# Optimization experiments

Measured on AMD Instinct MI355X. Metric: run time of the kernel, lower is better.

Reference implementation:

```python
import jax, jax.numpy as jnp
import numpy as np
import math

N_HEADS = 12  # from init_kwargs


def setup_inputs() -> dict:
    key = jax.random.key(0)
    ks = jax.random.split(key, 9)
    B, N, D = 32, 577, 768
    s = 1.0 / math.sqrt(D)
    return {
        "x": jax.random.normal(ks[0], (B, N, D), jnp.float32),
        "Wq": jax.random.normal(ks[1], (D, D), jnp.float32) * s,
        "bq": jax.random.normal(ks[2], (D,), jnp.float32) * 0.02,
        "Wk": jax.random.normal(ks[3], (D, D), jnp.float32) * s,
        "bk": jax.random.normal(ks[4], (D,), jnp.float32) * 0.02,
        "Wv": jax.random.normal(ks[5], (D, D), jnp.float32) * s,
        "bv": jax.random.normal(ks[6], (D,), jnp.float32) * 0.02,
        "Wo": jax.random.normal(ks[7], (D, D), jnp.float32) * s,
        "bo": jax.random.normal(ks[8], (D,), jnp.float32) * 0.02,
    }


def reference(x, Wq, bq, Wk, bk, Wv, bv, Wo, bo):
    B, N, D = x.shape
    H = N_HEADS
    Hd = D // H
    # project then split heads (intended semantics of the torch module)
    q = (x @ Wq.T + bq).reshape(B, N, H, Hd)
    k = (x @ Wk.T + bk).reshape(B, N, H, Hd)
    v = (x @ Wv.T + bv).reshape(B, N, H, Hd)
    # NOTE: faithful quirk - scale by sqrt(d_size), not sqrt(head_dim)
    scores = jnp.einsum('bqhd,bkhd->bhqk', q, k) / math.sqrt(D)  # [B,H,N,N]
    # faithful quirk: mask = triu(ones); positions where mask==0 (strictly
    # lower triangle, k < q) are filled with float32 min -> anti-causal mask
    allowed = jnp.triu(jnp.ones((N, N), dtype=bool))
    scores = jnp.where(allowed, scores, jnp.finfo(jnp.float32).min)
    att = jax.nn.softmax(scores, axis=3)  # dropout p=0.0 -> identity
    out = jnp.einsum('bhqk,bkhd->bqhd', att, v).reshape(B, N, D)
    return out @ Wo.T + bo
```

## Files before the change

### kernel.cpp

```cpp
#include <hip/hip_runtime.h>
#include <cstdint>
#include <cstddef>


typedef __bf16 bf16;
typedef __bf16 bf16x4 __attribute__((ext_vector_type(4)));
typedef __bf16 bf16x8 __attribute__((ext_vector_type(8)));
typedef float  f32x4  __attribute__((ext_vector_type(4)));

#define DEVI __device__ __forceinline__

constexpr int BATCH = 32;
constexpr int NSEQ  = 577;
constexpr int DMODEL= 768;
constexpr int NHEAD = 12;
constexpr int HD    = 64;
constexpr int M_ROWS = BATCH * NSEQ;
constexpr int M_PAD  = 145 * 128;
constexpr int N_PAD  = 640;
constexpr int QKV_N  = 3 * DMODEL;
constexpr float QSCALE = 0.036084391824351615f * 1.4426950408889634f;

DEVI void async_copy16(const void* g, void* l) {
  void* gg = (void*)(uintptr_t)g;
  __builtin_amdgcn_global_load_lds(
      (__attribute__((address_space(1))) void*)gg,
      (__attribute__((address_space(3))) void*)l,
      16, 0, 0);
}

DEVI f32x4 mfma16(bf16x8 a, bf16x8 b, f32x4 c) {
  return __builtin_amdgcn_mfma_f32_16x16x32_bf16(a, b, c, 0, 0, 0);
}

__global__ __launch_bounds__(256) void cast_kernel(
    const float* __restrict__ x,
    const float* __restrict__ wq, const float* __restrict__ wk,
    const float* __restrict__ wv, const float* __restrict__ wo,
    bf16* __restrict__ xb, bf16* __restrict__ wcat, bf16* __restrict__ wob)
{
  constexpr int XQ = (M_ROWS * DMODEL) / 4;
  constexpr int WQ = (DMODEL * DMODEL) / 4;
  int idx = blockIdx.x * 256 + threadIdx.x;
  const float4* src; bf16* dst; int off;
  if (idx < XQ) { src = (const float4*)x; dst = xb; off = idx; }
  else {
    int u = idx - XQ; int w = u / WQ; off = u - w * WQ;
    src = (const float4*)(w == 0 ? wq : w == 1 ? wk : w == 2 ? wv : wo);
    dst = (w < 3) ? (wcat + (size_t)w * DMODEL * DMODEL) : wob;
  }
  float4 v = src[off];
  bf16x4 o;
  o[0] = (bf16)v.x; o[1] = (bf16)v.y; o[2] = (bf16)v.z; o[3] = (bf16)v.w;
  *(bf16x4*)(dst + (size_t)off * 4) = o;
}

template <int MODE>
__global__ __launch_bounds__(256) void gemm_bt(
    const bf16* __restrict__ A, const bf16* __restrict__ Bw,
    const float* __restrict__ bias0, const float* __restrict__ bias1,
    const float* __restrict__ bias2,
    float* __restrict__ Cout,
    bf16* __restrict__ Qb, bf16* __restrict__ Kb, bf16* __restrict__ Vb)
{
  __shared__ __align__(16) char smem[65536];
  const int t = threadIdx.x;
  const int w = t >> 6, lane = t & 63;
  const int g = lane >> 4, cl = lane & 15;
  const int wm = (w >> 1) * 64, wn = (w & 1) * 64;

  constexpr int GX  = (MODE == 0 ? QKV_N : DMODEL) / 128;
  constexpr int NWG = GX * (M_PAD / 128);
  constexpr int QC  = NWG / 8, RC = NWG % 8;
  const int l   = blockIdx.y * GX + blockIdx.x;
  const int xcd = l & 7, pos = l >> 3;
  const int nl  = (xcd < RC ? xcd * (QC + 1) : RC * (QC + 1) + (xcd - RC) * QC) + pos;
  const int m0  = (nl / GX) * 128, n0 = (nl % GX) * 128;

  f32x4 acc[4][4] = {};

  const int srow = t >> 3;
  const int scol = ((t & 7) ^ (srow & 7)) * 8;
  const bf16* Ag = A  + (size_t)(m0 + srow) * 768 + scol;
  const bf16* Bg = Bw + (size_t)(n0 + srow) * 768 + scol;

  constexpr int NSTEP = 768 / 64;
  auto stage = [&](int st, int buf) {
    char* lA = smem + buf * 32768 + w * 1024;
    char* lB = smem + buf * 32768 + 16384 + w * 1024;
#pragma unroll
    for (int c = 0; c < 4; ++c) {
      async_copy16(Ag + st * 64 + (size_t)c * 32 * 768, lA + c * 4096);
      async_copy16(Bg + st * 64 + (size_t)c * 32 * 768, lB + c * 4096);
    }
  };

  stage(0, 0);
  stage(1, 1);

#pragma unroll
  for (int st = 0; st < NSTEP; ++st) {
    if (st < NSTEP - 1) asm volatile("s_waitcnt vmcnt(8)" ::: "memory");
    else                asm volatile("s_waitcnt vmcnt(0)" ::: "memory");
    asm volatile("s_barrier" ::: "memory");

    const int cur = st & 1;
    const bf16* As = (const bf16*)(smem + cur * 32768);
    const bf16* Bs = (const bf16*)(smem + cur * 32768 + 16384);
#pragma unroll
    for (int ks = 0; ks < 2; ++ks) {
      const int ch = ((ks * 4 + g) ^ (cl & 7)) * 8;
      bf16x8 af[4], bfr[4];
#pragma unroll
      for (int i = 0; i < 4; ++i)
        af[i] = *(const bf16x8*)(As + (wm + i * 16 + cl) * 64 + ch);
#pragma unroll
      for (int j = 0; j < 4; ++j)
        bfr[j] = *(const bf16x8*)(Bs + (wn + j * 16 + cl) * 64 + ch);
#pragma unroll
      for (int i = 0; i < 4; ++i)
#pragma unroll
        for (int j = 0; j < 4; ++j)
          acc[i][j] = mfma16(af[i], bfr[j], acc[i][j]);
    }
    asm volatile("s_barrier" ::: "memory");
    if (st + 2 < NSTEP) stage(st + 2, cur);
  }

  if constexpr (MODE == 0) {
    bf16* Cs = (bf16*)smem;
#pragma unroll
    for (int p = 0; p < 2; ++p) {
      __syncthreads();
      if ((w & 1) == p) {
#pragma unroll
        for (int j = 0; j < 4; ++j) {
          const int n = n0 + wn + j * 16 + cl;
          const int which = n >= 1536 ? 2 : (n >= 768 ? 1 : 0);
          const int rem = n - which * 768;
          const float bias =
              (which == 0 ? bias0 : which == 1 ? bias1 : bias2)[rem];
          const float sc = which == 0 ? QSCALE : 1.0f;
#pragma unroll
          for (int i = 0; i < 4; ++i)
#pragma unroll
            for (int r = 0; r < 4; ++r)
              Cs[(wm + i * 16 + g * 4 + r) * 72 + j * 16 + cl] =
                  (bf16)((acc[i][j][r] + bias) * sc);
        }
      }
      __syncthreads();
      const int nbase = n0 + p * 64;
      const int which = nbase >= 1536 ? 2 : (nbase >= 768 ? 1 : 0);
      const int rem0 = nbase - which * 768;
      const int h = rem0 >> 6;
      bf16* dst = which == 0 ? Qb : which == 1 ? Kb : Vb;
      const int row = t >> 1, colh = (t & 1) * 32;
      const unsigned m = (unsigned)(m0 + row);
      if (m < (unsigned)M_ROWS) {
        const unsigned bb = m / 577u;
        const unsigned nq = m - bb * 577u;
        bf16* dr = dst + ((size_t)(bb * NHEAD + h) * N_PAD + nq) * HD + colh;
        const bf16* sr = Cs + row * 72 + colh;
#pragma unroll
        for (int cc = 0; cc < 4; ++cc)
          *(bf16x8*)(dr + cc * 8) = *(const bf16x8*)(sr + cc * 8);
      }
    }
  } else {
#pragma unroll
    for (int j = 0; j < 4; ++j) {
      const int n = n0 + wn + j * 16 + cl;
      const float bias = bias0[n];
#pragma unroll
      for (int i = 0; i < 4; ++i) {
#pragma unroll
        for (int r = 0; r < 4; ++r) {
          const unsigned m = (unsigned)(m0 + wm + i * 16 + g * 4 + r);
          if (m < (unsigned)M_ROWS)
            Cout[(size_t)m * 768 + n] = acc[i][j][r] + bias;
        }
      }
    }
  }
}

__global__ __launch_bounds__(256) void transpose_v(
    const bf16* __restrict__ Vb, bf16* __restrict__ Vt)
{
  __shared__ __align__(16) bf16 Ls[64 * 72];
  const int t = threadIdx.x;
  const int bh = blockIdx.y, n0 = blockIdx.x * 64;

  const int nrow = n0 + (t >> 3);
  const bf16* src = Vb + ((size_t)bh * N_PAD + nrow) * HD + (t & 7) * 8;
  const bf16x8 z = {};
  bf16x8 a0 = (nrow      < NSEQ) ? *(const bf16x8*)src                      : z;
  bf16x8 a1 = (nrow + 32 < NSEQ) ? *(const bf16x8*)(src + (size_t)32 * HD)  : z;
  *(bf16x8*)(Ls + (t >> 3) * 72 + (t & 7) * 8) = a0;
  *(bf16x8*)(Ls + ((t >> 3) + 32) * 72 + (t & 7) * 8) = a1;
  __syncthreads();

  const int d = t >> 2, nc = (t & 3) * 16;
  bf16 o[16];
#pragma unroll
  for (int e = 0; e < 16; ++e) o[e] = Ls[(nc + e) * 72 + d];
  bf16* dst = Vt + ((size_t)bh * HD + d) * N_PAD + n0 + nc;
  *(bf16x8*)dst = *(bf16x8*)o;
  *(bf16x8*)(dst + 8) = *(bf16x8*)(o + 8);
}

__global__ __launch_bounds__(256) void attn_kernel(
    const bf16* __restrict__ Qb, const bf16* __restrict__ Kb,
    const bf16* __restrict__ Vtb, bf16* __restrict__ Ao)
{
  __shared__ __align__(16) bf16 Ks[2][64 * 64];
  __shared__ __align__(16) bf16 Vs[2][64 * 64];
  __shared__ __align__(16) bf16 Ps[4 * 32 * 64];

  const int t = threadIdx.x, w = t >> 6, lane = t & 63;
  const int g = lane >> 4, cl = lane & 15;
  const int qt = blockIdx.x;
  const int bh = blockIdx.y;
  const size_t kqbase = (size_t)bh * (N_PAD * HD);
  const size_t vbase  = (size_t)bh * (HD * N_PAD);

  const int srow = t >> 3;
  const int scol = ((t & 7) ^ (srow & 7)) * 8;

  const bf16* Kg = Kb  + kqbase + (size_t)srow * HD + scol;
  const bf16* Vg = Vtb + vbase  + (size_t)srow * N_PAD + scol;

  const int jb0 = 2 * qt, nit = 10 - jb0;

  bf16x8 aq[2][2];
#pragma unroll
  for (int ks = 0; ks < 2; ++ks)
#pragma unroll
    for (int f = 0; f < 2; ++f)
      aq[f][ks] = *(const bf16x8*)(
          Qb + kqbase + (size_t)(qt * 128 + w * 32 + f * 16 + cl) * HD +
          (ks * 4 + g) * 8);

#pragma unroll
  for (int c = 0; c < 2; ++c) {
    async_copy16(Kg + (size_t)(jb0 * 64 + c * 32) * HD,  (char*)Ks[0] + c * 4096 + w * 1024);
    async_copy16(Vg + jb0 * 64 + (size_t)(c * 32) * N_PAD, (char*)Vs[0] + c * 4096 + w * 1024);
  }
  __syncthreads();

  f32x4 oacc[2][4] = {};
  f32x4 lsum[2] = {};
  bf16x8 onesf;
#pragma unroll
  for (int e = 0; e < 8; ++e) onesf[e] = (bf16)(cl == 0 ? 1.0f : 0.0f);

  bf16* pw = Ps + w * 2048;
  const int qw0 = qt * 128 + w * 32;

  for (int it = 0; it < nit; ++it) {
    const int jb = jb0 + it;
    const int buf = it & 1;
    if (it + 1 < nit) {
      const int jn = jb + 1, nb = buf ^ 1;
#pragma unroll
      for (int c = 0; c < 2; ++c) {
        async_copy16(Kg + (size_t)(jn * 64 + c * 32) * HD,   (char*)Ks[nb] + c * 4096 + w * 1024);
        async_copy16(Vg + jn * 64 + (size_t)(c * 32) * N_PAD, (char*)Vs[nb] + c * 4096 + w * 1024);
      }
    }

    f32x4 s[2][4] = {};
    __builtin_amdgcn_s_setprio(1);
#pragma unroll
    for (int ks = 0; ks < 2; ++ks) {
      const int chk = ((ks * 4 + g) ^ (cl & 7)) * 8;
#pragma unroll
      for (int j = 0; j < 4; ++j) {
        bf16x8 bk = *(const bf16x8*)(Ks[buf] + (j * 16 + cl) * 64 + chk);
#pragma unroll
        for (int f = 0; f < 2; ++f)
          s[f][j] = mfma16(bk, aq[f][ks], s[f][j]);
      }
    }
    __builtin_amdgcn_s_setprio(0);

    float p[2][4][4];
    const bool need_mask = (jb * 64 < qw0 + 32) || (jb == 9);
    if (need_mask) {
#pragma unroll
      for (int f = 0; f < 2; ++f) {
        const int qglob = qw0 + f * 16 + cl;
#pragma unroll
        for (int j = 0; j < 4; ++j) {
#pragma unroll
          for (int r = 0; r < 4; ++r) {
            const int kg = jb * 64 + j * 16 + g * 4 + r;
            const bool ok = (kg >= qglob) && (kg < NSEQ);
            p[f][j][r] = ok ? exp2f(s[f][j][r]) : 0.f;
          }
        }
      }
    } else {
#pragma unroll
      for (int f = 0; f < 2; ++f)
#pragma unroll
        for (int j = 0; j < 4; ++j)
#pragma unroll
          for (int r = 0; r < 4; ++r)
            p[f][j][r] = exp2f(s[f][j][r]);
    }

#pragma unroll
    for (int f = 0; f < 2; ++f) {
      const int prow = f * 16 + cl;
      bf16* pr = pw + prow * 64;
      const int rk = prow & 7;
#pragma unroll
      for (int j = 0; j < 4; ++j) {
        const int c = j * 2 + (g >> 1);
        bf16x4 tmp;
#pragma unroll
        for (int r = 0; r < 4; ++r) tmp[r] = (bf16)p[f][j][r];
        *(bf16x4*)(pr + ((c ^ rk) * 8) + (g & 1) * 4) = tmp;
      }
    }

#pragma unroll
    for (int ks = 0; ks < 2; ++ks) {
      const int chp = ((ks * 4 + g) ^ (cl & 7)) * 8;
      bf16x8 ap[2], bv[4];
#pragma unroll
      for (int f = 0; f < 2; ++f)
        ap[f] = *(const bf16x8*)(pw + (f * 16 + cl) * 64 + chp);
#pragma unroll
      for (int j = 0; j < 4; ++j)
        bv[j] = *(const bf16x8*)(Vs[buf] + (j * 16 + cl) * 64 + chp);
      __builtin_amdgcn_s_setprio(1);
#pragma unroll
      for (int f = 0; f < 2; ++f) {
#pragma unroll
        for (int j = 0; j < 4; ++j)
          oacc[f][j] = mfma16(ap[f], bv[j], oacc[f][j]);
        lsum[f] = mfma16(ap[f], onesf, lsum[f]);
      }
      __builtin_amdgcn_s_setprio(0);
    }
    __syncthreads();
  }

  const int b_ = bh / NHEAD, h_ = bh - (bh / NHEAD) * NHEAD;
#pragma unroll
  for (int f = 0; f < 2; ++f)
#pragma unroll
    for (int r = 0; r < 4; ++r) {
      const int qg = qw0 + f * 16 + g * 4 + r;
      const float l = __shfl(lsum[f][r], lane & 48, 64);
      if (qg >= NSEQ) continue;
      const float inv = 1.f / l;
      const size_t row = ((size_t)b_ * NSEQ + qg) * DMODEL + h_ * HD;
#pragma unroll
      for (int j = 0; j < 4; ++j)
        Ao[row + j * 16 + cl] = (bf16)(oacc[f][j][r] * inv);
    }
}

extern "C" void kernel_launch(void* const* d_in, const int* in_sizes, int n_in,
                              void* d_out, int out_size, void* d_ws, size_t ws_size,
                              hipStream_t stream) {
  const float* x  = (const float*)d_in[0];
  const float* Wq = (const float*)d_in[1];
  const float* bq = (const float*)d_in[2];
  const float* Wk = (const float*)d_in[3];
  const float* bk = (const float*)d_in[4];
  const float* Wv = (const float*)d_in[5];
  const float* bv = (const float*)d_in[6];
  const float* Wo = (const float*)d_in[7];
  const float* bo = (const float*)d_in[8];

  char* ws = (char*)d_ws;
  size_t off = 0;
  auto alloc = [&](size_t bytes) -> char* {
    char* p = ws + off;
    off += (bytes + 255) & ~(size_t)255;
    return p;
  };
  bf16* xb   = (bf16*)alloc((size_t)M_PAD * DMODEL * 2);
  bf16* wcat = (bf16*)alloc((size_t)QKV_N * DMODEL * 2);
  bf16* wob  = (bf16*)alloc((size_t)DMODEL * DMODEL * 2);
  bf16* Qb   = (bf16*)alloc((size_t)BATCH * NHEAD * N_PAD * HD * 2);
  bf16* Kb   = (bf16*)alloc((size_t)BATCH * NHEAD * N_PAD * HD * 2);
  bf16* Vb   = (bf16*)alloc((size_t)BATCH * NHEAD * N_PAD * HD * 2);
  bf16* Vtb  = (bf16*)alloc((size_t)BATCH * NHEAD * HD * N_PAD * 2);
  bf16* Ao   = (bf16*)alloc((size_t)M_PAD * DMODEL * 2);
  (void)ws_size; (void)in_sizes; (void)n_in; (void)out_size;

  constexpr int XQ = (M_ROWS * DMODEL) / 4;
  constexpr int WQ = (DMODEL * DMODEL) / 4;
  const int cast_blocks = (XQ + 4 * WQ) / 256;
  cast_kernel<<<cast_blocks, 256, 0, stream>>>(x, Wq, Wk, Wv, Wo, xb, wcat, wob);

  gemm_bt<0><<<dim3(QKV_N / 128, M_PAD / 128), 256, 0, stream>>>(
      xb, wcat, bq, bk, bv, nullptr, Qb, Kb, Vb);

  transpose_v<<<dim3(N_PAD / 64, BATCH * NHEAD), 256, 0, stream>>>(Vb, Vtb);

  attn_kernel<<<dim3(5, BATCH * NHEAD), 256, 0, stream>>>(Qb, Kb, Vtb, Ao);

  gemm_bt<1><<<dim3(DMODEL / 128, M_PAD / 128), 256, 0, stream>>>(
      Ao, wob, bo, nullptr, nullptr, (float*)d_out, nullptr, nullptr, nullptr);
}
```

Before: 352.1 us.

## Load GEMM B operand directly into registers and halve LDS for occupancy

The GEMM no longer stages the weight (B) tile through shared memory. Each wave now double-buffers its B fragments in registers, read straight from global memory. Only the A tile stays in LDS, so the shared allocation drops from 64KB to 32KB and launch bounds ask for 3 blocks per CU. The goal is more resident blocks and less LDS traffic. In exchange, B global reads are less coalesced, B is fetched twice per block (once by each wave pair sharing a column slice), and register pressure rises.

```diff
diff --git a/kernel.cpp b/kernel.cpp
--- a/kernel.cpp
+++ b/kernel.cpp
@@ -56,14 +56,14 @@
 }
 
 template <int MODE>
-__global__ __launch_bounds__(256) void gemm_bt(
+__global__ __launch_bounds__(256, 3) void gemm_bt(
     const bf16* __restrict__ A, const bf16* __restrict__ Bw,
     const float* __restrict__ bias0, const float* __restrict__ bias1,
     const float* __restrict__ bias2,
     float* __restrict__ Cout,
     bf16* __restrict__ Qb, bf16* __restrict__ Kb, bf16* __restrict__ Vb)
 {
-  __shared__ __align__(16) char smem[65536];
+  __shared__ __align__(16) char smem[32768];
   const int t = threadIdx.x;
   const int w = t >> 6, lane = t & 63;
   const int g = lane >> 4, cl = lane & 15;
@@ -81,50 +81,60 @@
 
   const int srow = t >> 3;
   const int scol = ((t & 7) ^ (srow & 7)) * 8;
-  const bf16* Ag = A  + (size_t)(m0 + srow) * 768 + scol;
-  const bf16* Bg = Bw + (size_t)(n0 + srow) * 768 + scol;
+  const bf16* Ag = A + (size_t)(m0 + srow) * 768 + scol;
+
+  const bf16* Bg = Bw + (size_t)(n0 + wn + cl) * 768 + g * 8;
 
   constexpr int NSTEP = 768 / 64;
-  auto stage = [&](int st, int buf) {
-    char* lA = smem + buf * 32768 + w * 1024;
-    char* lB = smem + buf * 32768 + 16384 + w * 1024;
-#pragma unroll
-    for (int c = 0; c < 4; ++c) {
+  auto stageA = [&](int st, int buf) {
+    char* lA = smem + buf * 16384 + w * 1024;
+#pragma unroll
+    for (int c = 0; c < 4; ++c)
       async_copy16(Ag + st * 64 + (size_t)c * 32 * 768, lA + c * 4096);
-      async_copy16(Bg + st * 64 + (size_t)c * 32 * 768, lB + c * 4096);
-    }
   };
-
-  stage(0, 0);
-  stage(1, 1);
+  auto loadB = [&](int st, bf16x8 (&bb)[8]) {
+#pragma unroll
+    for (int ks = 0; ks < 2; ++ks)
+#pragma unroll
+      for (int j = 0; j < 4; ++j)
+        bb[ks * 4 + j] = *(const bf16x8*)(
+            Bg + (size_t)(j * 16) * 768 + st * 64 + ks * 32);
+  };
+  auto compute = [&](const bf16* As, bf16x8 (&bb)[8]) {
+#pragma unroll
+    for (int ks = 0; ks < 2; ++ks) {
+      const int ch = ((ks * 4 + g) ^ (cl & 7)) * 8;
+      bf16x8 af[4];
+#pragma unroll
+      for (int i = 0; i < 4; ++i)
+        af[i] = *(const bf16x8*)(As + (wm + i * 16 + cl) * 64 + ch);
+#pragma unroll
+      for (int i = 0; i < 4; ++i)
+#pragma unroll
+        for (int j = 0; j < 4; ++j)
+          acc[i][j] = mfma16(af[i], bb[ks * 4 + j], acc[i][j]);
+    }
+  };
+
+  bf16x8 bb0[8], bb1[8];
+  stageA(0, 0);
+  loadB(0, bb0);
+  stageA(1, 1);
 
 #pragma unroll
   for (int st = 0; st < NSTEP; ++st) {
-    if (st < NSTEP - 1) asm volatile("s_waitcnt vmcnt(8)" ::: "memory");
+    if (st < NSTEP - 1) asm volatile("s_waitcnt vmcnt(4)" ::: "memory");
     else                asm volatile("s_waitcnt vmcnt(0)" ::: "memory");
     asm volatile("s_barrier" ::: "memory");
 
-    const int cur = st & 1;
-    const bf16* As = (const bf16*)(smem + cur * 32768);
-    const bf16* Bs = (const bf16*)(smem + cur * 32768 + 16384);
-#pragma unroll
-    for (int ks = 0; ks < 2; ++ks) {
-      const int ch = ((ks * 4 + g) ^ (cl & 7)) * 8;
-      bf16x8 af[4], bfr[4];
-#pragma unroll
-      for (int i = 0; i < 4; ++i)
-        af[i] = *(const bf16x8*)(As + (wm + i * 16 + cl) * 64 + ch);
-#pragma unroll
-      for (int j = 0; j < 4; ++j)
-        bfr[j] = *(const bf16x8*)(Bs + (wn + j * 16 + cl) * 64 + ch);
-#pragma unroll
-      for (int i = 0; i < 4; ++i)
-#pragma unroll
-        for (int j = 0; j < 4; ++j)
-          acc[i][j] = mfma16(af[i], bfr[j], acc[i][j]);
-    }
+    const bf16* As = (const bf16*)(smem + (st & 1) * 16384);
+    if ((st & 1) == 0) compute(As, bb0); else compute(As, bb1);
+
     asm volatile("s_barrier" ::: "memory");
-    if (st + 2 < NSTEP) stage(st + 2, cur);
+    if (st + 1 < NSTEP) {
+      if ((st & 1) == 0) loadB(st + 1, bb1); else loadB(st + 1, bb0);
+    }
+    if (st + 2 < NSTEP) stageA(st + 2, st & 1);
   }
 
   if constexpr (MODE == 0) {
```

Result: slower. 429.7 us (+22.1%).
